# Performance work log

Measured on AMD Instinct MI355X. Metric: run time of the kernel, lower is better.

The kernel has to match this reference:

```python
import jax, jax.numpy as jnp
import numpy as np

B, S, D, H, KD, VD, HID, L, V, OUTN = 16, 512, 512, 8, 64, 64, 2048, 4, 32000, 128
EPS = 1e-5


def _layer_norm(x, g, b):
    m = jnp.mean(x, axis=-1, keepdims=True)
    v = jnp.mean(jnp.square(x - m), axis=-1, keepdims=True)
    return (x - m) * jax.lax.rsqrt(v + EPS) * g + b


def _pos_encoding(seq_len, d_model):
    pos = jnp.arange(seq_len, dtype=jnp.float32)[:, None]
    div = jnp.exp(jnp.arange(0, d_model, 2, dtype=jnp.float32) * (-np.log(10000.0) / d_model))
    pe = jnp.zeros((seq_len, d_model), dtype=jnp.float32)
    pe = pe.at[:, 0::2].set(jnp.sin(pos * div))
    pe = pe.at[:, 1::2].set(jnp.cos(pos * div))
    return pe


def setup_inputs() -> dict:
    key = jax.random.key(0)
    ks = jax.random.split(key, 32)
    s = 0.02
    n = jax.random.normal
    inp = {
        "enc_inputs": jax.random.randint(ks[0], (B, S), 0, V, dtype=jnp.int32),
        "emb": n(ks[1], (V, D), jnp.float32) * s,
        # stacked per-layer params, leading dim = L
        "Wq": n(ks[2], (L, D, H * KD), jnp.float32) * s,
        "bq": jnp.zeros((L, H * KD), jnp.float32),
        "Wk": n(ks[3], (L, D, H * KD), jnp.float32) * s,
        "bk": jnp.zeros((L, H * KD), jnp.float32),
        "Wv": n(ks[4], (L, D, H * VD), jnp.float32) * s,
        "bv": jnp.zeros((L, H * VD), jnp.float32),
        "Wo": n(ks[5], (L, H * VD, D), jnp.float32) * s,
        "bo": jnp.zeros((L, D), jnp.float32),
        "ln1_g": jnp.ones((L, D), jnp.float32),
        "ln1_b": jnp.zeros((L, D), jnp.float32),
        "W1": n(ks[6], (L, D, HID), jnp.float32) * s,   # conv1d k=1 == linear
        "b1": jnp.zeros((L, HID), jnp.float32),
        "W2": n(ks[7], (L, HID, D), jnp.float32) * s,
        "b2": jnp.zeros((L, D), jnp.float32),
        "ln2_g": jnp.ones((L, D), jnp.float32),
        "ln2_b": jnp.zeros((L, D), jnp.float32),
        # flatten head created inside torch forward: [S*D, 128]
        "Wf": n(ks[8], (S * D, OUTN), jnp.float32) * s,
        "bf": jnp.zeros((OUTN,), jnp.float32),
        "Wout": n(ks[9], (OUTN, 1), jnp.float32) * s,
        "bout": jnp.zeros((1,), jnp.float32),
    }
    return inp


def _encoder(enc_inputs, emb, Wq, bq, Wk, bk, Wv, bv, Wo, bo, ln1_g, ln1_b,
             W1, b1, W2, b2, ln2_g, ln2_b, Wf, bf, Wout, bout):
    x = emb[enc_inputs] + _pos_encoding(S, D)[None, :, :]          # [B,S,D]
    pad = (enc_inputs == 0)[:, None, None, :]                      # [B,1,1,S]
    scale = 1.0 / np.sqrt(D)                                       # note: sqrt(embed_dim), as in source
    for l in range(L):
        # multi-head attention
        q = (x @ Wq[l] + bq[l]).reshape(B, S, H, KD)
        k = (x @ Wk[l] + bk[l]).reshape(B, S, H, KD)
        v = (x @ Wv[l] + bv[l]).reshape(B, S, H, VD)
        scores = jnp.einsum('bqhd,bkhd->bhqk', q, k) * scale
        scores = jnp.where(pad, -1e9, scores)
        attn = jax.nn.softmax(scores, axis=-1)
        ctx = jnp.einsum('bhqk,bkhd->bqhd', attn, v).reshape(B, S, H * VD)
        x = _layer_norm(ctx @ Wo[l] + bo[l] + x, ln1_g[l], ln1_b[l])
        # position-wise FFN (conv1d kernel_size=1)
        h = jax.nn.relu(x @ W1[l] + b1[l])
        x = _layer_norm(h @ W2[l] + b2[l] + x, ln2_g[l], ln2_b[l])
    flat = x.reshape(B, S * D)
    features = flat @ Wf + bf                                      # [B,128]
    y_score = jax.nn.sigmoid(features @ Wout + bout)               # [B,1]
    y_pred = jnp.round(y_score)
    return y_score, y_pred, features


def reference(enc_inputs, emb, Wq, bq, Wk, bk, Wv, bv, Wo, bo, ln1_g, ln1_b,
              W1, b1, W2, b2, ln2_g, ln2_b, Wf, bf, Wout, bout):
    return _encoder(enc_inputs, emb, Wq, bq, Wk, bk, Wv, bv, Wo, bo, ln1_g, ln1_b,
                    W1, b1, W2, b2, ln2_g, ln2_b, Wf, bf, Wout, bout)
```

## Files before the change

kernel.cpp:

```cpp
#include <hip/hip_runtime.h>
#include <hip/hip_bf16.h>
#include <math.h>

typedef unsigned short ushort_t;
typedef __attribute__((ext_vector_type(8))) short bf16x8;
typedef __attribute__((ext_vector_type(4))) float f32x4;

#define SCALE_QK 0.04419417382415922f
#define PE_C 0.017988946039015986f

__device__ __forceinline__ void g2lds16(const void* g, void* l) {
    __builtin_amdgcn_global_load_lds(
        (const __attribute__((address_space(1))) unsigned int*)g,
        (__attribute__((address_space(3))) unsigned int*)l,
        16, 0, 0);
}
__device__ __forceinline__ ushort_t f2bs(float v) {
    __hip_bfloat16 h = __float2bfloat16(v);
    return *reinterpret_cast<ushort_t*>(&h);
}
__device__ __forceinline__ float bs2f(ushort_t v) {
    return __uint_as_float(((unsigned int)v) << 16);
}

template<bool RELU, bool VT>
__global__ __launch_bounds__(512, 2) void gemm8(
    const ushort_t* __restrict__ A, const ushort_t* __restrict__ B,
    const float* __restrict__ bias, ushort_t* __restrict__ C,
    ushort_t* __restrict__ vt, int K, int lda, int ldb, int ldc)
{
    __shared__ ushort_t As[2][256 * 64];
    __shared__ ushort_t Bs[2][256 * 64];

    const int t = threadIdx.x;
    const int lane = t & 63, w = t >> 6;
    const int l16 = lane & 15, quad = lane >> 4;
    const int r8 = lane >> 3;
    const int kg = ((lane & 7) ^ r8) << 3;
    const int wm = (w >> 2) * 128;
    const int wn = (w & 3) * 64;
    const int m0 = blockIdx.y * 256, n0 = blockIdx.x * 256;
    const int NT = K >> 6;

    f32x4 acc[8][4];
    #pragma unroll
    for (int i = 0; i < 8; i++)
        #pragma unroll
        for (int j = 0; j < 4; j++)
            acc[i][j] = (f32x4){0.f, 0.f, 0.f, 0.f};

    auto STAGE8 = [&](int kt, int bb) {
        int k0 = kt << 6;
        #pragma unroll
        for (int ii = 0; ii < 4; ii++) {
            int rbase = w * 32 + ii * 8;
            g2lds16(A + (size_t)(m0 + rbase + r8) * lda + k0 + kg,
                    &As[bb][rbase * 64]);
            g2lds16(B + (size_t)(n0 + rbase + r8) * ldb + k0 + kg,
                    &Bs[bb][rbase * 64]);
        }
    };

    STAGE8(0, 0);
    STAGE8(1, 1);

    for (int kt = 0; kt < NT; kt++) {
        const int bb = kt & 1;
        if (kt < NT - 1)
            asm volatile("s_waitcnt vmcnt(8)" ::: "memory");
        else
            asm volatile("s_waitcnt vmcnt(0)" ::: "memory");
        __builtin_amdgcn_s_barrier();
        asm volatile("" ::: "memory");

        #pragma unroll
        for (int tt = 0; tt < 2; tt++) {
            bf16x8 af[8], bf[4];
            #pragma unroll
            for (int i = 0; i < 8; i++) {
                int row = wm + i * 16 + l16;
                af[i] = *(const bf16x8*)&As[bb][row * 64 + ((((tt << 2) + quad) ^ (row & 7)) << 3)];
            }
            #pragma unroll
            for (int j = 0; j < 4; j++) {
                int row = wn + j * 16 + l16;
                bf[j] = *(const bf16x8*)&Bs[bb][row * 64 + ((((tt << 2) + quad) ^ (row & 7)) << 3)];
            }
            #pragma unroll
            for (int i = 0; i < 8; i++)
                #pragma unroll
                for (int j = 0; j < 4; j++)
                    acc[i][j] = __builtin_amdgcn_mfma_f32_16x16x32_bf16(
                        af[i], bf[j], acc[i][j], 0, 0, 0);
        }

        asm volatile("" ::: "memory");
        __builtin_amdgcn_s_barrier();
        asm volatile("" ::: "memory");
        if (kt + 2 < NT)
            STAGE8(kt + 2, bb);
    }

    if (VT && n0 >= 1024) {
        #pragma unroll
        for (int i = 0; i < 8; i++) {
            int mbase = m0 + wm + i * 16 + quad * 4;
            int b = mbase >> 9, s = mbase & 511;
            #pragma unroll
            for (int j = 0; j < 4; j++) {
                int n = n0 + wn + j * 16 + l16;
                int hv = n - 1024;
                int h = hv >> 6, vd = hv & 63;
                float bv = bias[n];
                ushort4 pk;
                pk.x = f2bs(acc[i][j][0] + bv);
                pk.y = f2bs(acc[i][j][1] + bv);
                pk.z = f2bs(acc[i][j][2] + bv);
                pk.w = f2bs(acc[i][j][3] + bv);
                *(ushort4*)&vt[((size_t)((b << 3) + h)) * 32768 + (size_t)vd * 512 + s] = pk;
            }
        }
        return;
    }

    #pragma unroll
    for (int i = 0; i < 8; i++)
        #pragma unroll
        for (int j = 0; j < 4; j++) {
            int n = n0 + wn + j * 16 + l16;
            float bv = bias[n];
            #pragma unroll
            for (int r = 0; r < 4; r++) {
                int m = m0 + wm + i * 16 + quad * 4 + r;
                float v = acc[i][j][r] + bv;
                if (RELU) v = fmaxf(v, 0.f);
                C[(size_t)m * ldc + n] = f2bs(v);
            }
        }
}

__global__ __launch_bounds__(256) void gemmLN(
    const ushort_t* __restrict__ A, const ushort_t* __restrict__ B,
    const float* __restrict__ bias, const ushort_t* __restrict__ res,
    const float* __restrict__ g, const float* __restrict__ bt,
    ushort_t* __restrict__ X, int K, int lda)
{
    __shared__ ushort_t As[2][32 * 64];
    __shared__ ushort_t Bs[2][512 * 64];
    __shared__ float2 pst[4][32];
    __shared__ float2 rmv[32];

    const int t = threadIdx.x;
    const int lane = t & 63, w = t >> 6;
    const int l16 = lane & 15, quad = lane >> 4;
    const int r8 = lane >> 3;
    const int kg = ((lane & 7) ^ r8) << 3;
    const int wn = w * 128;
    const int m0 = blockIdx.x * 32;
    const int NT = K >> 6;

    f32x4 acc[2][8];
    #pragma unroll
    for (int i = 0; i < 2; i++)
        #pragma unroll
        for (int j = 0; j < 8; j++)
            acc[i][j] = (f32x4){0.f, 0.f, 0.f, 0.f};

    auto STAGE = [&](int kt, int bb) {
        int k0 = kt << 6;
        g2lds16(A + (size_t)(m0 + w * 8 + r8) * lda + k0 + kg,
                &As[bb][(w * 8) * 64]);
        #pragma unroll
        for (int ii = 0; ii < 16; ii++) {
            int rbase = w * 128 + ii * 8;
            g2lds16(B + (size_t)(rbase + r8) * K + k0 + kg,
                    &Bs[bb][rbase * 64]);
        }
    };

    STAGE(0, 0);
    STAGE(1, 1);

    for (int kt = 0; kt < NT; kt++) {
        const int bb = kt & 1;
        if (kt < NT - 1)
            asm volatile("s_waitcnt vmcnt(17)" ::: "memory");
        else
            asm volatile("s_waitcnt vmcnt(0)" ::: "memory");
        __builtin_amdgcn_s_barrier();
        asm volatile("" ::: "memory");

        #pragma unroll
        for (int tt = 0; tt < 2; tt++) {
            bf16x8 af[2], bf8[8];
            #pragma unroll
            for (int i = 0; i < 2; i++) {
                int row = i * 16 + l16;
                af[i] = *(const bf16x8*)&As[bb][row * 64 + ((((tt << 2) + quad) ^ (row & 7)) << 3)];
            }
            #pragma unroll
            for (int j = 0; j < 8; j++) {
                int row = wn + j * 16 + l16;
                bf8[j] = *(const bf16x8*)&Bs[bb][row * 64 + ((((tt << 2) + quad) ^ (row & 7)) << 3)];
            }
            #pragma unroll
            for (int i = 0; i < 2; i++)
                #pragma unroll
                for (int j = 0; j < 8; j++)
                    acc[i][j] = __builtin_amdgcn_mfma_f32_16x16x32_bf16(
                        af[i], bf8[j], acc[i][j], 0, 0, 0);
        }

        asm volatile("" ::: "memory");
        __builtin_amdgcn_s_barrier();
        asm volatile("" ::: "memory");
        if (kt + 2 < NT)
            STAGE(kt + 2, bb);
    }

    float rs[2][4], rq[2][4];
    #pragma unroll
    for (int i = 0; i < 2; i++)
        #pragma unroll
        for (int r = 0; r < 4; r++) { rs[i][r] = 0.f; rq[i][r] = 0.f; }

    #pragma unroll
    for (int i = 0; i < 2; i++)
        #pragma unroll
        for (int j = 0; j < 8; j++) {
            int n = wn + j * 16 + l16;
            float bvn = bias[n];
            #pragma unroll
            for (int r = 0; r < 4; r++) {
                int row = i * 16 + quad * 4 + r;
                float v = acc[i][j][r] + bvn
                        + bs2f(res[(size_t)(m0 + row) * 512 + n]);
                acc[i][j][r] = v;
                rs[i][r] += v;
                rq[i][r] += v * v;
            }
        }

    #pragma unroll
    for (int i = 0; i < 2; i++)
        #pragma unroll
        for (int r = 0; r < 4; r++) {
            #pragma unroll
            for (int off = 1; off < 16; off <<= 1) {
                rs[i][r] += __shfl_xor(rs[i][r], off);
                rq[i][r] += __shfl_xor(rq[i][r], off);
            }
            if (l16 == 0)
                pst[w][i * 16 + quad * 4 + r] = make_float2(rs[i][r], rq[i][r]);
        }
    __syncthreads();
    if (t < 32) {
        float s = 0.f, q = 0.f;
        #pragma unroll
        for (int wv = 0; wv < 4; wv++) {
            float2 p = pst[wv][t];
            s += p.x; q += p.y;
        }
        float mean = s * (1.f / 512.f);
        float var = q * (1.f / 512.f) - mean * mean;
        rmv[t] = make_float2(mean, rsqrtf(var + 1e-5f));
    }
    __syncthreads();

    #pragma unroll
    for (int i = 0; i < 2; i++)
        #pragma unroll
        for (int j = 0; j < 8; j++) {
            int n = wn + j * 16 + l16;
            float gn = g[n], btn = bt[n];
            #pragma unroll
            for (int r = 0; r < 4; r++) {
                int row = i * 16 + quad * 4 + r;
                float2 mr = rmv[row];
                float o = (acc[i][j][r] - mr.x) * mr.y * gn + btn;
                X[(size_t)(m0 + row) * 512 + n] = f2bs(o);
            }
        }
}

__global__ __launch_bounds__(256) void flash_attn(
    ushort_t* __restrict__ QKV, const ushort_t* __restrict__ Vt,
    const int* __restrict__ tok)
{
    __shared__ ushort_t Qs[128 * 64];
    __shared__ ushort_t Ks[128 * 64];
    __shared__ ushort_t Vts[64 * 128];
    __shared__ ushort_t Ps[128 * 128];

    const int bh = blockIdx.y;
    const int b = bh >> 3, h = bh & 7;
    const int q0 = blockIdx.x * 128;
    const int t = threadIdx.x;
    const int lane = t & 63, w = t >> 6;
    const int l16 = lane & 15, quad = lane >> 4;
    const int wm = w * 32;
    const size_t rowbase = (size_t)b * 512;

    {
        int r8 = lane >> 3;
        int kg = (lane & 7) ^ r8;
        #pragma unroll
        for (int ii = 0; ii < 4; ii++) {
            int rb = w * 32 + ii * 8;
            g2lds16(QKV + (rowbase + q0 + rb + r8) * 1536 + h * 64 + kg * 8,
                    &Qs[rb * 64]);
        }
    }

    f32x4 accO[2][4];
    #pragma unroll
    for (int i = 0; i < 2; i++)
        #pragma unroll
        for (int jv = 0; jv < 4; jv++)
            accO[i][jv] = (f32x4){0.f, 0.f, 0.f, 0.f};
    float lrow[2][4];
    #pragma unroll
    for (int i = 0; i < 2; i++)
        #pragma unroll
        for (int r = 0; r < 4; r++) lrow[i][r] = 0.f;

    for (int kc = 0; kc < 4; kc++) {
        __syncthreads();
        {
            int r8 = lane >> 3;
            int kg = (lane & 7) ^ r8;
            #pragma unroll
            for (int ii = 0; ii < 4; ii++) {
                int rb = w * 32 + ii * 8;
                g2lds16(QKV + (rowbase + kc * 128 + rb + r8) * 1536 + 512 + h * 64 + kg * 8,
                        &Ks[rb * 64]);
            }
        }
        {
            int v4 = lane >> 4;
            #pragma unroll
            for (int ii = 0; ii < 4; ii++) {
                int vb = w * 16 + ii * 4;
                int vd = vb + v4;
                int kg = (lane & 15) ^ (vd & 15);
                g2lds16(Vt + (size_t)bh * 32768 + (size_t)vd * 512 + kc * 128 + kg * 8,
                        &Vts[vb * 128]);
            }
        }
        float maskv[8];
        #pragma unroll
        for (int j = 0; j < 8; j++)
            maskv[j] = (tok[b * 512 + kc * 128 + j * 16 + l16] == 0) ? -1e9f : 0.f;

        __syncthreads();

        f32x4 sacc[2][8];
        #pragma unroll
        for (int i = 0; i < 2; i++)
            #pragma unroll
            for (int j = 0; j < 8; j++)
                sacc[i][j] = (f32x4){0.f, 0.f, 0.f, 0.f};
        #pragma unroll
        for (int tt = 0; tt < 2; tt++) {
            bf16x8 aq[2], bk8[8];
            #pragma unroll
            for (int i = 0; i < 2; i++) {
                int row = wm + i * 16 + l16;
                aq[i] = *(const bf16x8*)&Qs[row * 64 + (((tt << 2) + quad) ^ (row & 7)) * 8];
            }
            #pragma unroll
            for (int j = 0; j < 8; j++) {
                int row = j * 16 + l16;
                bk8[j] = *(const bf16x8*)&Ks[row * 64 + (((tt << 2) + quad) ^ (row & 7)) * 8];
            }
            #pragma unroll
            for (int i = 0; i < 2; i++)
                #pragma unroll
                for (int j = 0; j < 8; j++)
                    sacc[i][j] = __builtin_amdgcn_mfma_f32_16x16x32_bf16(
                        aq[i], bk8[j], sacc[i][j], 0, 0, 0);
        }

        #pragma unroll
        for (int i = 0; i < 2; i++)
            #pragma unroll
            for (int j = 0; j < 8; j++)
                #pragma unroll
                for (int r = 0; r < 4; r++) {
                    float p = __expf(fmaf(sacc[i][j][r], SCALE_QK, maskv[j]));
                    sacc[i][j][r] = p;
                    lrow[i][r] += p;
                }

        #pragma unroll
        for (int i = 0; i < 2; i++)
            #pragma unroll
            for (int j = 0; j < 8; j++) {
                int col = j * 16 + l16;
                int colc = col >> 3, csub = col & 7;
                #pragma unroll
                for (int r = 0; r < 4; r++) {
                    int row = wm + i * 16 + quad * 4 + r;
                    Ps[row * 128 + ((colc ^ (row & 15)) << 3) + csub] = f2bs(sacc[i][j][r]);
                }
            }

        #pragma unroll
        for (int tt = 0; tt < 4; tt++) {
            bf16x8 ap[2], bv8[4];
            #pragma unroll
            for (int i = 0; i < 2; i++) {
                int row = wm + i * 16 + l16;
                ap[i] = *(const bf16x8*)&Ps[row * 128 + ((((tt << 2) + quad)) ^ (row & 15)) * 8];
            }
            #pragma unroll
            for (int jv = 0; jv < 4; jv++) {
                int vd = jv * 16 + l16;
                bv8[jv] = *(const bf16x8*)&Vts[vd * 128 + (((tt << 2) + quad) ^ (vd & 15)) * 8];
            }
            #pragma unroll
            for (int i = 0; i < 2; i++)
                #pragma unroll
                for (int jv = 0; jv < 4; jv++)
                    accO[i][jv] = __builtin_amdgcn_mfma_f32_16x16x32_bf16(
                        ap[i], bv8[jv], accO[i][jv], 0, 0, 0);
        }
    }

    #pragma unroll
    for (int i = 0; i < 2; i++)
        #pragma unroll
        for (int r = 0; r < 4; r++) {
            float s = lrow[i][r];
            #pragma unroll
            for (int off = 1; off < 16; off <<= 1)
                s += __shfl_xor(s, off);
            float inv = 1.f / s;
            int row = q0 + wm + i * 16 + quad * 4 + r;
            #pragma unroll
            for (int jv = 0; jv < 4; jv++) {
                int vd = jv * 16 + l16;
                QKV[(rowbase + row) * 1536 + h * 64 + vd] = f2bs(accO[i][jv][r] * inv);
            }
        }
}

__global__ __launch_bounds__(256) void prep(
    const float* __restrict__ Wq, const float* __restrict__ Wk,
    const float* __restrict__ Wv, const float* __restrict__ Wo,
    const float* __restrict__ W1, const float* __restrict__ W2,
    const float* __restrict__ bq, const float* __restrict__ bk,
    const float* __restrict__ bv, const int* __restrict__ tok,
    const float* __restrict__ emb,
    __hip_bfloat16* __restrict__ WqkvT, __hip_bfloat16* __restrict__ WoT,
    __hip_bfloat16* __restrict__ W1T, __hip_bfloat16* __restrict__ W2T,
    float* __restrict__ bqkv, float* __restrict__ Fb,
    __hip_bfloat16* __restrict__ xb)
{
    const int blk = blockIdx.x;
    const int t = threadIdx.x;

    if (blk < 12288) {
        __shared__ float tile[32][33];
        const float* in; __hip_bfloat16* out;
        long long inz, outz; int R, Cc, bx, by, bz;
        if (blk < 4096) {
            int seg = blk >> 10, lb = blk & 1023;
            bz = lb >> 8; by = (lb >> 4) & 15; bx = lb & 15;
            R = 512; Cc = 512; inz = 262144;
            if      (seg == 0) { in = Wq; out = WqkvT;          outz = 786432; }
            else if (seg == 1) { in = Wk; out = WqkvT + 262144; outz = 786432; }
            else if (seg == 2) { in = Wv; out = WqkvT + 524288; outz = 786432; }
            else               { in = Wo; out = WoT;            outz = 262144; }
        } else if (blk < 8192) {
            int lb = blk - 4096;
            bz = lb >> 10; by = (lb >> 6) & 15; bx = lb & 63;
            R = 512; Cc = 2048; inz = 1048576; outz = 1048576;
            in = W1; out = W1T;
        } else {
            int lb = blk - 8192;
            bz = lb >> 10; by = (lb >> 4) & 63; bx = lb & 15;
            R = 2048; Cc = 512; inz = 1048576; outz = 1048576;
            in = W2; out = W2T;
        }
        in += bz * inz; out += bz * outz;
        int c0 = bx * 32, r0 = by * 32;
        int tx = t & 31, ty = t >> 5;
        #pragma unroll
        for (int i = 0; i < 4; i++)
            tile[ty + i * 8][tx] = in[(size_t)(r0 + ty + i * 8) * Cc + c0 + tx];
        __syncthreads();
        #pragma unroll
        for (int i = 0; i < 4; i++)
            out[(size_t)(c0 + ty + i * 8) * R + r0 + tx] =
                __float2bfloat16(tile[tx][ty + i * 8]);
    } else if (blk < 12312) {
        int k = blk - 12288;
        int idx = k * 256 + t;
        int l = idx / 1536, n = idx - l * 1536;
        float v = (n < 512) ? bq[l * 512 + n]
                : (n < 1024) ? bk[l * 512 + n - 512]
                             : bv[l * 512 + n - 1024];
        bqkv[idx] = v;
        if (k < 8) Fb[k * 256 + t] = 0.f;
    } else {
        int idx = (blk - 12312) * 256 + t;
        int d  = idx & 511;
        int bs = idx >> 9;
        int s  = bs & 511;
        int tk = tok[bs];
        float freq  = expf(-(float)(d & ~1) * PE_C);
        float angle = (float)s * freq;
        float pe    = (d & 1) ? cosf(angle) : sinf(angle);
        xb[idx] = __float2bfloat16(emb[(size_t)tk * 512 + d] + pe);
    }
}

__global__ __launch_bounds__(256) void feat_partial(const ushort_t* __restrict__ Xb,
                                                    const float* __restrict__ Wf,
                                                    float* __restrict__ Fb) {
    int slice = blockIdx.x;
    int k0 = slice * 512;
    __shared__ float Xs[16][512];
    __shared__ float Red[2048];
    int t = threadIdx.x;
    for (int i = t; i < 2048; i += 256) {
        int b = i >> 7, c4 = (i & 127) * 4;
        ushort4 u = *(const ushort4*)&Xb[(size_t)b * 262144 + k0 + c4];
        Xs[b][c4 + 0] = bs2f(u.x);
        Xs[b][c4 + 1] = bs2f(u.y);
        Xs[b][c4 + 2] = bs2f(u.z);
        Xs[b][c4 + 3] = bs2f(u.w);
        Red[i] = 0.f;
    }
    __syncthreads();
    int n4 = (t & 31) * 4;
    int kh = t >> 5;
    float4 acc[16];
    #pragma unroll
    for (int b = 0; b < 16; b++) acc[b] = (float4){0.f, 0.f, 0.f, 0.f};
    for (int kk4 = 0; kk4 < 16; kk4++) {
        int kb = kh * 64 + kk4 * 4;
        float4 w0 = *(const float4*)&Wf[(size_t)(k0 + kb + 0) * 128 + n4];
        float4 w1 = *(const float4*)&Wf[(size_t)(k0 + kb + 1) * 128 + n4];
        float4 w2 = *(const float4*)&Wf[(size_t)(k0 + kb + 2) * 128 + n4];
        float4 w3 = *(const float4*)&Wf[(size_t)(k0 + kb + 3) * 128 + n4];
        #pragma unroll
        for (int b = 0; b < 16; b++) {
            float4 xq = *(const float4*)&Xs[b][kb];
            acc[b].x += xq.x * w0.x + xq.y * w1.x + xq.z * w2.x + xq.w * w3.x;
            acc[b].y += xq.x * w0.y + xq.y * w1.y + xq.z * w2.y + xq.w * w3.y;
            acc[b].z += xq.x * w0.z + xq.y * w1.z + xq.z * w2.z + xq.w * w3.z;
            acc[b].w += xq.x * w0.w + xq.y * w1.w + xq.z * w2.w + xq.w * w3.w;
        }
    }
    #pragma unroll
    for (int b = 0; b < 16; b++) {
        atomicAdd(&Red[b * 128 + n4 + 0], acc[b].x);
        atomicAdd(&Red[b * 128 + n4 + 1], acc[b].y);
        atomicAdd(&Red[b * 128 + n4 + 2], acc[b].z);
        atomicAdd(&Red[b * 128 + n4 + 3], acc[b].w);
    }
    __syncthreads();
    for (int o = t; o < 2048; o += 256)
        atomicAdd(&Fb[o], Red[o]);
}

__global__ __launch_bounds__(256) void head_kernel(const float* __restrict__ feat,
                                                   const float* __restrict__ bfv,
                                                   const float* __restrict__ Wo2,
                                                   const float* __restrict__ bo2,
                                                   float* __restrict__ out) {
    __shared__ float f[2048];
    int t = threadIdx.x;
    for (int i = t; i < 2048; i += 256) {
        float v = feat[i] + bfv[i & 127];
        f[i] = v;
        out[32 + i] = v;
    }
    __syncthreads();
    if (t < 16) {
        float zv = bo2[0];
        for (int n = 0; n < 128; n++) zv = fmaf(f[t * 128 + n], Wo2[n], zv);
        float ys = 1.f / (1.f + expf(-zv));
        out[t] = ys;
        out[16 + t] = rintf(ys);
    }
}

extern "C" void kernel_launch(void* const* d_in, const int* in_sizes, int n_in,
                              void* d_out, int out_size, void* d_ws, size_t ws_size,
                              hipStream_t stream) {
    const int*   enc  = (const int*)  d_in[0];
    const float* emb  = (const float*)d_in[1];
    const float* Wq   = (const float*)d_in[2];
    const float* bq   = (const float*)d_in[3];
    const float* Wk   = (const float*)d_in[4];
    const float* bk   = (const float*)d_in[5];
    const float* Wv   = (const float*)d_in[6];
    const float* bv   = (const float*)d_in[7];
    const float* Wo   = (const float*)d_in[8];
    const float* bo   = (const float*)d_in[9];
    const float* g1   = (const float*)d_in[10];
    const float* be1  = (const float*)d_in[11];
    const float* W1   = (const float*)d_in[12];
    const float* b1f  = (const float*)d_in[13];
    const float* W2   = (const float*)d_in[14];
    const float* b2f  = (const float*)d_in[15];
    const float* g2   = (const float*)d_in[16];
    const float* be2  = (const float*)d_in[17];
    const float* Wf   = (const float*)d_in[18];
    const float* bf   = (const float*)d_in[19];
    const float* Wout = (const float*)d_in[20];
    const float* bout = (const float*)d_in[21];
    float* out = (float*)d_out;

    char* ws = (char*)d_ws;
    ushort_t* Xb   = (ushort_t*) (ws + 16777216);
    ushort_t* QKV  = (ushort_t*) (ws + 25165824);
    ushort_t* Vt   = (ushort_t*) (ws + 50331648);
    ushort_t* S    = (ushort_t*) (ws + 58720256);
    ushort_t* WqkvT= (ushort_t*) (ws + 92274688);
    ushort_t* WoT  = (ushort_t*) (ws + 98566144);
    ushort_t* W1T  = (ushort_t*) (ws + 100663296);
    ushort_t* W2T  = (ushort_t*) (ws + 109051904);
    float*    bqkv = (float*)    (ws + 117440512);
    float*    Fb   = (float*)    (ws + 117465088);

    typedef __hip_bfloat16 bf16;

    prep<<<28696, 256, 0, stream>>>(
        Wq, Wk, Wv, Wo, W1, W2, bq, bk, bv, enc, emb,
        (bf16*)WqkvT, (bf16*)WoT, (bf16*)W1T, (bf16*)W2T, bqkv, Fb, (bf16*)Xb);

    for (int l = 0; l < 4; l++) {
        gemm8<false, true><<<dim3(6, 32), 512, 0, stream>>>(
            Xb, WqkvT + (size_t)l * 786432, bqkv + l * 1536,
            QKV, Vt, 512, 512, 512, 1536);

        flash_attn<<<dim3(4, 128), 256, 0, stream>>>(QKV, Vt, enc);

        gemmLN<<<256, 256, 0, stream>>>(
            QKV, WoT + (size_t)l * 262144, bo + l * 512, Xb,
            g1 + l * 512, be1 + l * 512, Xb, 512, 1536);

        gemm8<true, false><<<dim3(8, 32), 512, 0, stream>>>(
            Xb, W1T + (size_t)l * 1048576, b1f + l * 2048,
            S, nullptr, 512, 512, 512, 2048);

        gemmLN<<<256, 256, 0, stream>>>(
            S, W2T + (size_t)l * 1048576, b2f + l * 512, Xb,
            g2 + l * 512, be2 + l * 512, Xb, 2048, 2048);
    }

    feat_partial<<<512, 256, 0, stream>>>(Xb, Wf, Fb);
    head_kernel<<<1, 256, 0, stream>>>(Fb, bf, Wout, bout, out);
}
```

Baseline: 987.9 us.

## Double gemmLN waves per block and split feature GEMV across more blocks

```diff
diff --git a/kernel.cpp b/kernel.cpp
--- a/kernel.cpp
+++ b/kernel.cpp
@@ -139,7 +139,7 @@
         }
 }
 
-__global__ __launch_bounds__(256) void gemmLN(
+__global__ __launch_bounds__(512) void gemmLN(
     const ushort_t* __restrict__ A, const ushort_t* __restrict__ B,
     const float* __restrict__ bias, const ushort_t* __restrict__ res,
     const float* __restrict__ g, const float* __restrict__ bt,
@@ -147,7 +147,7 @@
 {
     __shared__ ushort_t As[2][32 * 64];
     __shared__ ushort_t Bs[2][512 * 64];
-    __shared__ float2 pst[4][32];
+    __shared__ float2 pst[8][32];
     __shared__ float2 rmv[32];
 
     const int t = threadIdx.x;
@@ -155,24 +155,25 @@
     const int l16 = lane & 15, quad = lane >> 4;
     const int r8 = lane >> 3;
     const int kg = ((lane & 7) ^ r8) << 3;
-    const int wn = w * 128;
+    const int wn = w * 64;
     const int m0 = blockIdx.x * 32;
     const int NT = K >> 6;
 
-    f32x4 acc[2][8];
-    #pragma unroll
-    for (int i = 0; i < 2; i++)
-        #pragma unroll
-        for (int j = 0; j < 8; j++)
+    f32x4 acc[2][4];
+    #pragma unroll
+    for (int i = 0; i < 2; i++)
+        #pragma unroll
+        for (int j = 0; j < 4; j++)
             acc[i][j] = (f32x4){0.f, 0.f, 0.f, 0.f};
 
     auto STAGE = [&](int kt, int bb) {
         int k0 = kt << 6;
-        g2lds16(A + (size_t)(m0 + w * 8 + r8) * lda + k0 + kg,
-                &As[bb][(w * 8) * 64]);
-        #pragma unroll
-        for (int ii = 0; ii < 16; ii++) {
-            int rbase = w * 128 + ii * 8;
+        if (w < 4)
+            g2lds16(A + (size_t)(m0 + w * 8 + r8) * lda + k0 + kg,
+                    &As[bb][(w * 8) * 64]);
+        #pragma unroll
+        for (int ii = 0; ii < 8; ii++) {
+            int rbase = w * 64 + ii * 8;
             g2lds16(B + (size_t)(rbase + r8) * K + k0 + kg,
                     &Bs[bb][rbase * 64]);
         }
@@ -183,32 +184,34 @@
 
     for (int kt = 0; kt < NT; kt++) {
         const int bb = kt & 1;
-        if (kt < NT - 1)
-            asm volatile("s_waitcnt vmcnt(17)" ::: "memory");
-        else
+        if (kt < NT - 1) {
+            if (w < 4) asm volatile("s_waitcnt vmcnt(9)" ::: "memory");
+            else       asm volatile("s_waitcnt vmcnt(8)" ::: "memory");
+        } else {
             asm volatile("s_waitcnt vmcnt(0)" ::: "memory");
+        }
         __builtin_amdgcn_s_barrier();
         asm volatile("" ::: "memory");
 
         #pragma unroll
         for (int tt = 0; tt < 2; tt++) {
-            bf16x8 af[2], bf8[8];
+            bf16x8 af[2], bf4[4];
             #pragma unroll
             for (int i = 0; i < 2; i++) {
                 int row = i * 16 + l16;
                 af[i] = *(const bf16x8*)&As[bb][row * 64 + ((((tt << 2) + quad) ^ (row & 7)) << 3)];
             }
             #pragma unroll
-            for (int j = 0; j < 8; j++) {
+            for (int j = 0; j < 4; j++) {
                 int row = wn + j * 16 + l16;
-                bf8[j] = *(const bf16x8*)&Bs[bb][row * 64 + ((((tt << 2) + quad) ^ (row & 7)) << 3)];
+                bf4[j] = *(const bf16x8*)&Bs[bb][row * 64 + ((((tt << 2) + quad) ^ (row & 7)) << 3)];
             }
             #pragma unroll
             for (int i = 0; i < 2; i++)
                 #pragma unroll
-                for (int j = 0; j < 8; j++)
+                for (int j = 0; j < 4; j++)
                     acc[i][j] = __builtin_amdgcn_mfma_f32_16x16x32_bf16(
-                        af[i], bf8[j], acc[i][j], 0, 0, 0);
+                        af[i], bf4[j], acc[i][j], 0, 0, 0);
         }
 
         asm volatile("" ::: "memory");
@@ -227,7 +230,7 @@
     #pragma unroll
     for (int i = 0; i < 2; i++)
         #pragma unroll
-        for (int j = 0; j < 8; j++) {
+        for (int j = 0; j < 4; j++) {
             int n = wn + j * 16 + l16;
             float bvn = bias[n];
             #pragma unroll
@@ -257,7 +260,7 @@
     if (t < 32) {
         float s = 0.f, q = 0.f;
         #pragma unroll
-        for (int wv = 0; wv < 4; wv++) {
+        for (int wv = 0; wv < 8; wv++) {
             float2 p = pst[wv][t];
             s += p.x; q += p.y;
         }
@@ -270,7 +273,7 @@
     #pragma unroll
     for (int i = 0; i < 2; i++)
         #pragma unroll
-        for (int j = 0; j < 8; j++) {
+        for (int j = 0; j < 4; j++) {
             int n = wn + j * 16 + l16;
             float gn = g[n], btn = bt[n];
             #pragma unroll
@@ -519,41 +522,56 @@
 __global__ __launch_bounds__(256) void feat_partial(const ushort_t* __restrict__ Xb,
                                                     const float* __restrict__ Wf,
                                                     float* __restrict__ Fb) {
-    int slice = blockIdx.x;
-    int k0 = slice * 512;
-    __shared__ float Xs[16][512];
+    const int slice = blockIdx.x;
+    const int k0 = slice * 128;
+    __shared__ float Xs[16][128];
     __shared__ float Red[2048];
-    int t = threadIdx.x;
-    for (int i = t; i < 2048; i += 256) {
-        int b = i >> 7, c4 = (i & 127) * 4;
+    const int t = threadIdx.x;
+
+    #pragma unroll
+    for (int i = 0; i < 2; i++) {
+        int idx = t + i * 256;
+        int b = idx >> 5, c4 = (idx & 31) * 4;
         ushort4 u = *(const ushort4*)&Xb[(size_t)b * 262144 + k0 + c4];
         Xs[b][c4 + 0] = bs2f(u.x);
         Xs[b][c4 + 1] = bs2f(u.y);
         Xs[b][c4 + 2] = bs2f(u.z);
         Xs[b][c4 + 3] = bs2f(u.w);
-        Red[i] = 0.f;
-    }
+    }
+    #pragma unroll
+    for (int i = 0; i < 8; i++) Red[t + i * 256] = 0.f;
     __syncthreads();
-    int n4 = (t & 31) * 4;
-    int kh = t >> 5;
+
+    const int n4 = (t & 31) * 4;
+    const int kh = t >> 5;
+    const int rbase = kh * 16;
+    const float* wp = Wf + (size_t)(k0 + rbase) * 128 + n4;
+
     float4 acc[16];
     #pragma unroll
     for (int b = 0; b < 16; b++) acc[b] = (float4){0.f, 0.f, 0.f, 0.f};
-    for (int kk4 = 0; kk4 < 16; kk4++) {
-        int kb = kh * 64 + kk4 * 4;
-        float4 w0 = *(const float4*)&Wf[(size_t)(k0 + kb + 0) * 128 + n4];
-        float4 w1 = *(const float4*)&Wf[(size_t)(k0 + kb + 1) * 128 + n4];
-        float4 w2 = *(const float4*)&Wf[(size_t)(k0 + kb + 2) * 128 + n4];
-        float4 w3 = *(const float4*)&Wf[(size_t)(k0 + kb + 3) * 128 + n4];
+
+    #pragma unroll
+    for (int half = 0; half < 2; half++) {
+        float4 wv[8];
+        #pragma unroll
+        for (int kk = 0; kk < 8; kk++)
+            wv[kk] = *(const float4*)&wp[(size_t)(half * 8 + kk) * 128];
         #pragma unroll
         for (int b = 0; b < 16; b++) {
-            float4 xq = *(const float4*)&Xs[b][kb];
-            acc[b].x += xq.x * w0.x + xq.y * w1.x + xq.z * w2.x + xq.w * w3.x;
-            acc[b].y += xq.x * w0.y + xq.y * w1.y + xq.z * w2.y + xq.w * w3.y;
-            acc[b].z += xq.x * w0.z + xq.y * w1.z + xq.z * w2.z + xq.w * w3.z;
-            acc[b].w += xq.x * w0.w + xq.y * w1.w + xq.z * w2.w + xq.w * w3.w;
-        }
-    }
+            float4 x0 = *(const float4*)&Xs[b][rbase + half * 8];
+            float4 x1 = *(const float4*)&Xs[b][rbase + half * 8 + 4];
+            acc[b].x += x0.x*wv[0].x + x0.y*wv[1].x + x0.z*wv[2].x + x0.w*wv[3].x
+                      + x1.x*wv[4].x + x1.y*wv[5].x + x1.z*wv[6].x + x1.w*wv[7].x;
+            acc[b].y += x0.x*wv[0].y + x0.y*wv[1].y + x0.z*wv[2].y + x0.w*wv[3].y
+                      + x1.x*wv[4].y + x1.y*wv[5].y + x1.z*wv[6].y + x1.w*wv[7].y;
+            acc[b].z += x0.x*wv[0].z + x0.y*wv[1].z + x0.z*wv[2].z + x0.w*wv[3].z
+                      + x1.x*wv[4].z + x1.y*wv[5].z + x1.z*wv[6].z + x1.w*wv[7].z;
+            acc[b].w += x0.x*wv[0].w + x0.y*wv[1].w + x0.z*wv[2].w + x0.w*wv[3].w
+                      + x1.x*wv[4].w + x1.y*wv[5].w + x1.z*wv[6].w + x1.w*wv[7].w;
+        }
+    }
+
     #pragma unroll
     for (int b = 0; b < 16; b++) {
         atomicAdd(&Red[b * 128 + n4 + 0], acc[b].x);
@@ -562,8 +580,11 @@
         atomicAdd(&Red[b * 128 + n4 + 3], acc[b].w);
     }
     __syncthreads();
-    for (int o = t; o < 2048; o += 256)
+    #pragma unroll
+    for (int i = 0; i < 8; i++) {
+        int o = t + i * 256;
         atomicAdd(&Fb[o], Red[o]);
+    }
 }
 
 __global__ __launch_bounds__(256) void head_kernel(const float* __restrict__ feat,
@@ -640,7 +661,7 @@
 
         flash_attn<<<dim3(4, 128), 256, 0, stream>>>(QKV, Vt, enc);
 
-        gemmLN<<<256, 256, 0, stream>>>(
+        gemmLN<<<256, 512, 0, stream>>>(
             QKV, WoT + (size_t)l * 262144, bo + l * 512, Xb,
             g1 + l * 512, be1 + l * 512, Xb, 512, 1536);
 
@@ -648,11 +669,11 @@
             Xb, W1T + (size_t)l * 1048576, b1f + l * 2048,
             S, nullptr, 512, 512, 512, 2048);
 
-        gemmLN<<<256, 256, 0, stream>>>(
+        gemmLN<<<256, 512, 0, stream>>>(
             S, W2T + (size_t)l * 1048576, b2f + l * 512, Xb,
             g2 + l * 512, be2 + l * 512, Xb, 2048, 2048);
     }
 
-    feat_partial<<<512, 256, 0, stream>>>(Xb, Wf, Fb);
+    feat_partial<<<2048, 256, 0, stream>>>(Xb, Wf, Fb);
     head_kernel<<<1, 256, 0, stream>>>(Fb, bf, Wout, bout, out);
 }
```

After: 1.037 ms. +5.0%, slower.
